# Optimization experiments

Measured on AMD Instinct MI355X. Metric: run time of the kernel, lower is better.

Reference implementation:

```python
import jax, jax.numpy as jnp
import numpy as np

N, NFEAT, NHID, NCLASS, NIDX = 200000, 512, 128, 70, 10000


def normalize_l2(X):
    # row L2-normalize; norm is detached in the original (stop_gradient),
    # inf scale (zero rows) mapped to 0
    rownorm = jax.lax.stop_gradient(jnp.linalg.norm(X, axis=1, keepdims=True))
    scale = jnp.where(rownorm > 0, 1.0 / rownorm, 0.0)
    return X * scale


def setup_inputs() -> dict:
    key = jax.random.key(0)
    ks = jax.random.split(key, 9)
    x = jax.random.normal(ks[0], (N, NFEAT), dtype=jnp.float32)
    simple_features = jax.random.normal(ks[1], (N, NFEAT), dtype=jnp.float32)
    idx = jax.random.randint(ks[2], (NIDX,), 0, N)
    s = 0.05
    W0 = jax.random.normal(ks[3], (NHID, NFEAT), dtype=jnp.float32) * s
    W1 = jax.random.normal(ks[4], (NHID, NFEAT), dtype=jnp.float32) * s
    G1 = jax.random.normal(ks[5], (NHID, NHID), dtype=jnp.float32) * s
    G2 = jax.random.normal(ks[6], (NHID, NHID), dtype=jnp.float32) * s
    GT = jax.random.normal(ks[7], (NHID, 2 * NHID), dtype=jnp.float32) * s
    Wc = jax.random.normal(ks[8], (NCLASS, NHID), dtype=jnp.float32) * s
    return {"x": x, "simple_features": simple_features, "idx": idx,
            "W0": W0, "W1": W1, "G1": G1, "G2": G2, "GT": GT, "Wc": Wc}


def reference(x, simple_features, idx, W0, W1, G1, G2, GT, Wc):
    x = normalize_l2(x)                      # [N, nfeat]
    sf = normalize_l2(simple_features)       # [N, nfeat]
    # dropout/dropout_adj are identity (p=0)
    layer_inner = jax.nn.relu(x @ W0.T)      # [N, nhid]
    lay_simple = jax.nn.relu(sf @ W1.T)      # [N, nhid]
    gate1 = layer_inner @ G1.T               # [N, nhid]
    gate2 = lay_simple @ G2.T                # [N, nhid]
    gate = jax.nn.sigmoid(jnp.concatenate([gate1, gate2], axis=1) @ GT.T)
    fix_inner = (1.0 - gate) * layer_inner + gate * lay_simple
    fix_inner = normalize_l2(fix_inner)
    logits = jax.nn.relu(fix_inner @ Wc.T)   # [N, nclass]
    return jax.nn.log_softmax(logits, axis=-1)[idx]
```

## Files before the change

### kernel.cpp

```cpp
#include <hip/hip_runtime.h>
#include <math.h>

#define NFEAT  512
#define NHID   128
#define NCLASS 70
#define NIDX   10000
#define NTILE  625
#define NT2    313
#define HELEMS (2u * NIDX * NHID)
#define GELEMS (2u * NIDX * NHID)
#define WIMG_ELEMS (2u * 128 * 512)
#define SMALL_ELEMS 74496u
#define WS_NEED ((size_t)(HELEMS + GELEMS + WIMG_ELEMS + SMALL_ELEMS) * 2)

typedef float  f32x4  __attribute__((ext_vector_type(4)));
typedef __bf16 bf16x8 __attribute__((ext_vector_type(8)));

static __device__ __forceinline__ unsigned short f2bf(float f) {
    unsigned u = __builtin_bit_cast(unsigned, f);
    u += 0x7fffu + ((u >> 16) & 1u);
    return (unsigned short)(u >> 16);
}
static __device__ __forceinline__ float bf2f(unsigned short h) {
    unsigned u = ((unsigned)h) << 16;
    return __builtin_bit_cast(float, u);
}
static __device__ __forceinline__ bf16x8 pack8(float4 a, float4 b) {
    bf16x8 r;
    r[0] = (__bf16)a.x; r[1] = (__bf16)a.y; r[2] = (__bf16)a.z; r[3] = (__bf16)a.w;
    r[4] = (__bf16)b.x; r[5] = (__bf16)b.y; r[6] = (__bf16)b.z; r[7] = (__bf16)b.w;
    return r;
}
static __device__ __forceinline__ bf16x8 pack8s(float4 a, float4 b, float s) {
    bf16x8 r;
    r[0] = (__bf16)(a.x * s); r[1] = (__bf16)(a.y * s); r[2] = (__bf16)(a.z * s); r[3] = (__bf16)(a.w * s);
    r[4] = (__bf16)(b.x * s); r[5] = (__bf16)(b.y * s); r[6] = (__bf16)(b.z * s); r[7] = (__bf16)(b.w * s);
    return r;
}
static __device__ __forceinline__ f32x4 MFMA(bf16x8 a, bf16x8 b, f32x4 c) {
    return __builtin_amdgcn_mfma_f32_16x16x32_bf16(a, b, c, 0, 0, 0);
}
static __device__ __forceinline__ bf16x8 ldsAx(const unsigned short* base, int row, int colb, int rstride) {
    return *(const bf16x8*)((const char*)base + row * rstride + (colb ^ ((row & 7) << 4)));
}
static __device__ __forceinline__ void ldsW1(unsigned short* base, int row, int col, unsigned short v) {
    *(unsigned short*)((char*)base + row * 256 + ((col * 2) ^ ((row & 7) << 4))) = v;
}
static __device__ __forceinline__ float ldsR1(const unsigned short* base, int row, int col) {
    return bf2f(*(const unsigned short*)((const char*)base + row * 256 + ((col * 2) ^ ((row & 7) << 4))));
}

__global__ void prep_weights(const float* __restrict__ W0, const float* __restrict__ W1,
                             const float* __restrict__ G1, const float* __restrict__ G2,
                             const float* __restrict__ GT, const float* __restrict__ Wc,
                             unsigned short* __restrict__ wsWimg,
                             unsigned short* __restrict__ wsSmall) {
    int i = blockIdx.x * 256 + threadIdx.x;
    if (i < 16384) {
        int t = i >> 13;
        int r = i & 8191;
        int n = r >> 6, k8 = r & 63;
        const float* src = (t ? W1 : W0) + (size_t)n * NFEAT + k8 * 8;
        float4 a = ((const float4*)src)[0], b = ((const float4*)src)[1];
        char* dst = (char*)wsWimg + t * 131072 + n * 1024 + ((k8 * 16) ^ ((n & 7) << 4));
        *(bf16x8*)dst = pack8(a, b);
    } else {
        int i4 = i - 16384;
        if (i4 >= 18624) return;
        const float* src; int base4, dstb;
        if      (i4 < 4096)  { src = G1; base4 = 0;     dstb = 0; }
        else if (i4 < 8192)  { src = G2; base4 = 4096;  dstb = 16384; }
        else if (i4 < 16384) { src = GT; base4 = 8192;  dstb = 32768; }
        else                 { src = Wc; base4 = 16384; dstb = 65536; }
        float4 v = ((const float4*)src)[i4 - base4];
        ushort4 o;
        o.x = f2bf(v.x); o.y = f2bf(v.y); o.z = f2bf(v.z); o.w = f2bf(v.w);
        *(ushort4*)(wsSmall + dstb + (size_t)(i4 - base4) * 4) = o;
    }
}

__global__ __launch_bounds__(512) void stageBC(
    const float* __restrict__ x, const float* __restrict__ sf,
    const int* __restrict__ idx,
    const unsigned short* __restrict__ wsWimg,
    const unsigned short* __restrict__ wsSmall,
    unsigned short* __restrict__ wsH,
    unsigned short* __restrict__ wsG)
{
    __shared__ __align__(16) unsigned short Wl[65536];
    __shared__ __align__(16) unsigned short Xl[8192];
    __shared__ __align__(16) unsigned short Hl[2048];
    __shared__ __align__(16) unsigned short Gl[2048];

    const int tid  = threadIdx.x;
    const int w    = tid >> 6;
    const int lane = tid & 63;
    const int ln   = lane & 15, lg = lane >> 4;
    const int bid  = blockIdx.x;
    const int t    = bid / 125, tb = bid % 125;
    const int tile0 = tb * 5;
    const float* XS = t ? sf : x;
    const f32x4 zero4 = {0.f, 0.f, 0.f, 0.f};

    float4 ga0, ga1, gb0, gb1;
    {
        int r0 = idx[tile0 * 16 + w];
        int r1 = idx[tile0 * 16 + w + 8];
        const float4* p0 = (const float4*)(XS + (size_t)r0 * NFEAT + lane * 8);
        const float4* p1 = (const float4*)(XS + (size_t)r1 * NFEAT + lane * 8);
        ga0 = p0[0]; ga1 = p0[1];
        gb0 = p1[0]; gb1 = p1[1];
    }
    bf16x8 cf[4];
    {
        const unsigned short* Gsm = wsSmall + t * 16384;
        #pragma unroll
        for (int kc = 0; kc < 4; ++kc)
            cf[kc] = *(const bf16x8*)(Gsm + (size_t)(w * 16 + ln) * NHID + kc * 32 + lg * 8);
    }
    {
        const uint4* src = (const uint4*)((const char*)wsWimg + (size_t)t * 131072);
        uint4* dst = (uint4*)Wl;
        #pragma unroll
        for (int i = 0; i < 16; ++i) dst[tid + i * 512] = src[tid + i * 512];
    }
    auto putX = [&](int m, float4 a, float4 b) {
        float ss = a.x*a.x + a.y*a.y + a.z*a.z + a.w*a.w
                 + b.x*b.x + b.y*b.y + b.z*b.z + b.w*b.w;
        #pragma unroll
        for (int d = 1; d < 64; d <<= 1) ss += __shfl_xor(ss, d);
        float scl = (ss > 0.f) ? (1.f / sqrtf(ss)) : 0.f;
        *(bf16x8*)((char*)Xl + m * 1024 + ((lane * 16) ^ ((m & 7) << 4))) = pack8s(a, b, scl);
    };
    putX(w,     ga0, ga1);
    putX(w + 8, gb0, gb1);
    __syncthreads();

    for (int it = 0; it < 5; ++it) {
        float4 na0, na1, nb0, nb1;
        if (it < 4) {
            int tile = tile0 + it + 1;
            int r0 = idx[tile * 16 + w];
            int r1 = idx[tile * 16 + w + 8];
            const float4* p0 = (const float4*)(XS + (size_t)r0 * NFEAT + lane * 8);
            const float4* p1 = (const float4*)(XS + (size_t)r1 * NFEAT + lane * 8);
            na0 = p0[0]; na1 = p0[1];
            nb0 = p1[0]; nb1 = p1[1];
        }
        f32x4 accE = zero4, accO = zero4;
        #pragma unroll
        for (int kc = 0; kc < 16; ++kc) {
            bf16x8 a = ldsAx(Xl, ln,          kc * 64 + lg * 16, 1024);
            bf16x8 b = ldsAx(Wl, w * 16 + ln, kc * 64 + lg * 16, 1024);
            if (kc & 1) accO = MFMA(a, b, accO); else accE = MFMA(a, b, accE);
        }
        f32x4 acc = accE + accO;
        #pragma unroll
        for (int rg = 0; rg < 4; ++rg)
            ldsW1(Hl, lg * 4 + rg, w * 16 + ln, f2bf(fmaxf(acc[rg], 0.f)));
        __syncthreads();

        f32x4 aC = zero4;
        #pragma unroll
        for (int kc = 0; kc < 4; ++kc) {
            bf16x8 a = ldsAx(Hl, ln, kc * 64 + lg * 16, 256);
            aC = MFMA(a, cf[kc], aC);
        }
        if (tid < 256) {
            int tile = tile0 + it;
            ((uint4*)(wsH + ((size_t)t * NIDX + (size_t)tile * 16) * NHID))[tid]
                = ((const uint4*)Hl)[tid];
        }
        if (it < 4) {
            putX(w,     na0, na1);
            putX(w + 8, nb0, nb1);
        }
        #pragma unroll
        for (int rg = 0; rg < 4; ++rg)
            ldsW1(Gl, lg * 4 + rg, w * 16 + ln, f2bf(aC[rg]));
        __syncthreads();

        if (tid < 256) {
            int tile = tile0 + it;
            ((uint4*)(wsG + ((size_t)t * NIDX + (size_t)tile * 16) * NHID))[tid]
                = ((const uint4*)Gl)[tid];
        }
    }
}

__global__ __launch_bounds__(512) void tailDE2(
    const unsigned short* __restrict__ wsSmall,
    const unsigned short* __restrict__ wsH,
    const unsigned short* __restrict__ wsG,
    float* __restrict__ out)
{
    __shared__ __align__(16) unsigned short Hbuf[2][2][16][NHID];
    __shared__ __align__(16) unsigned short G12s[2][2][16][NHID];
    __shared__ __align__(16) unsigned short FIXs[2][16][NHID];
    __shared__ float scl2[2][16];

    const unsigned short* GTp = wsSmall + 32768;
    const unsigned short* Wcp = wsSmall + 65536;

    const int tid  = threadIdx.x;
    const int bid  = blockIdx.x;
    const int w    = tid >> 6;
    const int lane = tid & 63;
    const int ln   = lane & 15, lg = lane >> 4;
    const f32x4 zero4 = {0.f, 0.f, 0.f, 0.f};
    const int tile0 = bid * 2;
    const int tiles[2] = { tile0, (tile0 + 1 < NTILE) ? tile0 + 1 : NTILE - 1 };

    #pragma unroll
    for (int i = 0; i < 2; ++i) {
        int q = tid + i * 512;
        int seg = q >> 8, r = q & 255;
        int ti = seg >> 1, tt = seg & 1;
        size_t off = ((size_t)tt * NIDX + (size_t)tiles[ti] * 16) * NHID;
        ((uint4*)&Hbuf[0][0][0][0])[q] = ((const uint4*)(wsH + off))[r];
        ((uint4*)&G12s[0][0][0][0])[q] = ((const uint4*)(wsG + off))[r];
    }
    const int nD = w * 16 + ln;
    bf16x8 gt[8];
    #pragma unroll
    for (int kc = 0; kc < 8; ++kc)
        gt[kc] = *(const bf16x8*)(GTp + (size_t)nD * (2 * NHID) + kc * 32 + lg * 8);
    const int ccE = w * 16 + ln;
    const int ccl = (ccE < NCLASS) ? ccE : 0;
    bf16x8 wcf[4];
    #pragma unroll
    for (int kc = 0; kc < 4; ++kc)
        wcf[kc] = *(const bf16x8*)(Wcp + (size_t)ccl * NHID + kc * 32 + lg * 8);
    __syncthreads();

    #pragma unroll
    for (int ti = 0; ti < 2; ++ti) {
        f32x4 aE = zero4, aO = zero4;
        #pragma unroll
        for (int kc = 0; kc < 8; ++kc) {
            const unsigned short* As = &G12s[ti][kc >> 2][0][0];
            bf16x8 a = ldsAx(As, ln, (kc & 3) * 64 + lg * 16, 256);
            if (kc & 1) aO = MFMA(a, gt[kc], aO); else aE = MFMA(a, gt[kc], aE);
        }
        f32x4 accD = aE + aO;
        #pragma unroll
        for (int rg = 0; rg < 4; ++rg) {
            int m = lg * 4 + rg;
            float g  = 1.f / (1.f + __expf(-accD[rg]));
            float h0 = ldsR1(&Hbuf[ti][0][0][0], m, nD);
            float h1 = ldsR1(&Hbuf[ti][1][0][0], m, nD);
            ldsW1(&FIXs[ti][0][0], m, nD, f2bf((1.f - g) * h0 + g * h1));
        }
    }
    __syncthreads();

    {
        int rr = tid >> 4, sl = tid & 15;
        int ti = rr >> 4, r = rr & 15;
        bf16x8 v = ldsAx(&FIXs[ti][0][0], r, sl * 16, 256);
        float ss = 0.f;
        #pragma unroll
        for (int j = 0; j < 8; ++j) { float f = (float)v[j]; ss += f * f; }
        ss += __shfl_xor(ss, 1); ss += __shfl_xor(ss, 2);
        ss += __shfl_xor(ss, 4); ss += __shfl_xor(ss, 8);
        if (sl == 0) scl2[ti][r] = (ss > 0.f) ? (1.f / sqrtf(ss)) : 0.f;
    }
    __syncthreads();

    if (w < 5) {
        const bool live = (ccE < NCLASS);
        bf16x8 bfz;
        #pragma unroll
        for (int j = 0; j < 8; ++j) bfz[j] = (__bf16)0.f;
        #pragma unroll
        for (int ti = 0; ti < 2; ++ti) {
            f32x4 accE = zero4;
            #pragma unroll
            for (int kc = 0; kc < 4; ++kc) {
                bf16x8 a = ldsAx(&FIXs[ti][0][0], ln, kc * 64 + lg * 16, 256);
                accE = MFMA(a, live ? wcf[kc] : bfz, accE);
            }
            if (live) {
                float* LO = (float*)((char*)&G12s[0][0][0][0] + ti * 8192);
                #pragma unroll
                for (int rg = 0; rg < 4; ++rg) {
                    int m = lg * 4 + rg;
                    LO[m * 80 + ccE] = fmaxf(accE[rg] * scl2[ti][m], 0.f);
                }
            }
        }
    }
    __syncthreads();

    {
        int rr = tid >> 4, l16 = tid & 15;
        int ti = rr >> 4, r = rr & 15;
        const float* LO = (const float*)((const char*)&G12s[0][0][0][0] + ti * 8192) + r * 80;
        float v[5];
        #pragma unroll
        for (int j = 0; j < 5; ++j) {
            int c = l16 + j * 16;
            v[j] = (c < NCLASS) ? LO[c] : -1e30f;
        }
        float mx = v[0];
        #pragma unroll
        for (int j = 1; j < 5; ++j) mx = fmaxf(mx, v[j]);
        mx = fmaxf(mx, __shfl_xor(mx, 1)); mx = fmaxf(mx, __shfl_xor(mx, 2));
        mx = fmaxf(mx, __shfl_xor(mx, 4)); mx = fmaxf(mx, __shfl_xor(mx, 8));
        float se = 0.f;
        #pragma unroll
        for (int j = 0; j < 5; ++j) {
            int c = l16 + j * 16;
            if (c < NCLASS) se += __expf(v[j] - mx);
        }
        se += __shfl_xor(se, 1); se += __shfl_xor(se, 2);
        se += __shfl_xor(se, 4); se += __shfl_xor(se, 8);
        float lz = mx + __logf(se);
        int tile = tile0 + ti;
        if (tile < NTILE) {
            size_t orow = (size_t)tile * 16 + r;
            #pragma unroll
            for (int j = 0; j < 5; ++j) {
                int c = l16 + j * 16;
                if (c < NCLASS) out[orow * NCLASS + c] = v[j] - lz;
            }
        }
    }
}

static __device__ __forceinline__ bf16x8 bfragF(const float* p, size_t off) {
    const float4* q = (const float4*)(p + off);
    return pack8(q[0], q[1]);
}
__global__ __launch_bounds__(512) void hyper_fb(
    const float* __restrict__ x, const float* __restrict__ sf,
    const int* __restrict__ idx,
    const float* __restrict__ W0, const float* __restrict__ W1,
    const float* __restrict__ G1, const float* __restrict__ G2,
    const float* __restrict__ GT, const float* __restrict__ Wc,
    float* __restrict__ out)
{
    __shared__ __align__(16) unsigned short Xbuf[2][16][NFEAT];
    __shared__ __align__(16) unsigned short Hbuf[2][16][NHID];
    __shared__ float scl2[16];
    unsigned short* G12 = &Xbuf[0][0][0];
    unsigned short* FIX = &Xbuf[0][0][0] + 4096;
    float*          LOG = (float*)(&Xbuf[0][0][0] + 6144);

    const int tid = threadIdx.x, bid = blockIdx.x;
    const int w = tid >> 6, lane = tid & 63;
    const int ln = lane & 15, lg = lane >> 4;
    const int tB = w >> 2, nq = w & 3;
    const f32x4 zero4 = {0.f, 0.f, 0.f, 0.f};

    {
        char* xb = (char*)&Xbuf[0][0][0];
        #pragma unroll
        for (int j = 0; j < 4; ++j) {
            int p = w * 4 + j, t = p >> 4, m = p & 15;
            int ri = idx[bid * 16 + m];
            const float4* q = (const float4*)((t ? sf : x) + (size_t)ri * NFEAT + lane * 8);
            float4 a = q[0], b = q[1];
            float ss = a.x*a.x + a.y*a.y + a.z*a.z + a.w*a.w
                     + b.x*b.x + b.y*b.y + b.z*b.z + b.w*b.w;
            #pragma unroll
            for (int d = 1; d < 64; d <<= 1) ss += __shfl_xor(ss, d);
            float scl = (ss > 0.f) ? (1.f / sqrtf(ss)) : 0.f;
            int soff = t * 16384 + m * 1024 + ((lane * 16) ^ ((m & 7) << 4));
            *(bf16x8*)(xb + soff) = pack8s(a, b, scl);
        }
    }
    __syncthreads();
    {
        const float* Wp = tB ? W1 : W0;
        f32x4 acc0 = zero4, acc1 = zero4;
        const unsigned short* Xb = (const unsigned short*)((const char*)&Xbuf[0][0][0] + tB * 16384);
        #pragma unroll
        for (int kc = 0; kc < 16; ++kc) {
            bf16x8 a = ldsAx(Xb, ln, kc * 64 + lg * 16, 1024);
            acc0 = MFMA(a, bfragF(Wp, (size_t)(nq * 32 + ln) * NFEAT + kc * 32 + lg * 8), acc0);
            acc1 = MFMA(a, bfragF(Wp, (size_t)(nq * 32 + 16 + ln) * NFEAT + kc * 32 + lg * 8), acc1);
        }
        unsigned short* Hb = &Hbuf[tB][0][0];
        #pragma unroll
        for (int rg = 0; rg < 4; ++rg) {
            int m = lg * 4 + rg;
            ldsW1(Hb, m, nq * 32 + ln,      f2bf(fmaxf(acc0[rg], 0.f)));
            ldsW1(Hb, m, nq * 32 + 16 + ln, f2bf(fmaxf(acc1[rg], 0.f)));
        }
    }
    __syncthreads();
    {
        const float* Gp = tB ? G2 : G1;
        const unsigned short* Hs = &Hbuf[tB][0][0];
        f32x4 accC[2] = {zero4, zero4};
        #pragma unroll
        for (int kc = 0; kc < 4; ++kc) {
            bf16x8 a = ldsAx(Hs, ln, kc * 64 + lg * 16, 256);
            accC[0] = MFMA(a, bfragF(Gp, (size_t)(nq * 32 + ln) * NHID + kc * 32 + lg * 8), accC[0]);
            accC[1] = MFMA(a, bfragF(Gp, (size_t)(nq * 32 + 16 + ln) * NHID + kc * 32 + lg * 8), accC[1]);
        }
        unsigned short* Gd = G12 + tB * 2048;
        #pragma unroll
        for (int nt = 0; nt < 2; ++nt)
            #pragma unroll
            for (int rg = 0; rg < 4; ++rg) {
                int m = lg * 4 + rg;
                ldsW1(Gd, m, nq * 32 + nt * 16 + ln, f2bf(accC[nt][rg]));
            }
    }
    __syncthreads();
    {
        f32x4 accD = zero4;
        const int n = w * 16 + ln;
        #pragma unroll
        for (int kc = 0; kc < 8; ++kc) {
            const unsigned short* As = G12 + (kc >> 2) * 2048;
            bf16x8 a = ldsAx(As, ln, (kc & 3) * 64 + lg * 16, 256);
            accD = MFMA(a, bfragF(GT, (size_t)n * (2 * NHID) + kc * 32 + lg * 8), accD);
        }
        #pragma unroll
        for (int rg = 0; rg < 4; ++rg) {
            int m = lg * 4 + rg;
            float g  = 1.f / (1.f + __expf(-accD[rg]));
            float h0 = ldsR1(&Hbuf[0][0][0], m, n);
            float h1 = ldsR1(&Hbuf[1][0][0], m, n);
            ldsW1(FIX, m, n, f2bf((1.f - g) * h0 + g * h1));
        }
    }
    __syncthreads();
    if (tid < 256) {
        int r = tid >> 4, sl = tid & 15;
        bf16x8 v = ldsAx(FIX, r, sl * 16, 256);
        float ss = 0.f;
        #pragma unroll
        for (int j = 0; j < 8; ++j) { float f = (float)v[j]; ss += f * f; }
        ss += __shfl_xor(ss, 1); ss += __shfl_xor(ss, 2);
        ss += __shfl_xor(ss, 4); ss += __shfl_xor(ss, 8);
        if (sl == 0) scl2[r] = (ss > 0.f) ? (1.f / sqrtf(ss)) : 0.f;
    }
    __syncthreads();
    if (w < 5) {
        const int cc = w * 16 + ln;
        bf16x8 bfz;
        #pragma unroll
        for (int j = 0; j < 8; ++j) bfz[j] = (__bf16)0.f;
        f32x4 accE = zero4;
        #pragma unroll
        for (int kc = 0; kc < 4; ++kc) {
            bf16x8 a = ldsAx(FIX, ln, kc * 64 + lg * 16, 256);
            bf16x8 b = (cc < NCLASS) ? bfragF(Wc, (size_t)cc * NHID + kc * 32 + lg * 8) : bfz;
            accE = MFMA(a, b, accE);
        }
        #pragma unroll
        for (int rg = 0; rg < 4; ++rg) {
            int m = lg * 4 + rg;
            float v = fmaxf(accE[rg] * scl2[m], 0.f);
            LOG[m * 80 + cc] = (cc < NCLASS) ? v : -1e30f;
        }
    }
    __syncthreads();
    {
        const int r = tid >> 5, l32 = tid & 31;
        float v0 = LOG[r * 80 + l32];
        float v1 = LOG[r * 80 + 32 + l32];
        float v2 = (l32 < 16) ? LOG[r * 80 + 64 + l32] : -1e30f;
        float mx = fmaxf(fmaxf(v0, v1), v2);
        #pragma unroll
        for (int d = 1; d < 32; d <<= 1) mx = fmaxf(mx, __shfl_xor(mx, d, 32));
        float se = __expf(v0 - mx) + __expf(v1 - mx) + ((l32 < 16) ? __expf(v2 - mx) : 0.f);
        #pragma unroll
        for (int d = 1; d < 32; d <<= 1) se += __shfl_xor(se, d, 32);
        float lz = mx + __logf(se);
        size_t orow = (size_t)bid * 16 + r;
        out[orow * NCLASS + l32] = v0 - lz;
        if (l32 + 32 < NCLASS) out[orow * NCLASS + 32 + l32] = v1 - lz;
        if (l32 + 64 < NCLASS) out[orow * NCLASS + 64 + l32] = v2 - lz;
    }
}

extern "C" void kernel_launch(void* const* d_in, const int* in_sizes, int n_in,
                              void* d_out, int out_size, void* d_ws, size_t ws_size,
                              hipStream_t stream)
{
    const float* x   = (const float*)d_in[0];
    const float* sf  = (const float*)d_in[1];
    const int*   idx = (const int*)d_in[2];
    const float* W0  = (const float*)d_in[3];
    const float* W1  = (const float*)d_in[4];
    const float* G1  = (const float*)d_in[5];
    const float* G2  = (const float*)d_in[6];
    const float* GT  = (const float*)d_in[7];
    const float* Wc  = (const float*)d_in[8];
    float* out = (float*)d_out;

    if (ws_size >= WS_NEED) {
        unsigned short* wsH     = (unsigned short*)d_ws;
        unsigned short* wsG     = wsH + HELEMS;
        unsigned short* wsWimg  = wsG + GELEMS;
        unsigned short* wsSmall = wsWimg + WIMG_ELEMS;
        prep_weights<<<dim3(137), dim3(256), 0, stream>>>(W0, W1, G1, G2, GT, Wc, wsWimg, wsSmall);
        stageBC<<<dim3(250), dim3(512), 0, stream>>>(x, sf, idx, wsWimg, wsSmall, wsH, wsG);
        tailDE2<<<dim3(NT2), dim3(512), 0, stream>>>(wsSmall, wsH, wsG, out);
    } else {
        hyper_fb<<<dim3(NTILE), dim3(512), 0, stream>>>(
            x, sf, idx, W0, W1, G1, G2, GT, Wc, out);
    }
}
```

Before: 36.95 us.

## Fuse tail stage into stageBC via last-arriver atomic counter per tile group

```diff
diff --git a/kernel.cpp b/kernel.cpp
--- a/kernel.cpp
+++ b/kernel.cpp
@@ -6,12 +6,12 @@
 #define NCLASS 70
 #define NIDX   10000
 #define NTILE  625
-#define NT2    313
 #define HELEMS (2u * NIDX * NHID)
 #define GELEMS (2u * NIDX * NHID)
 #define WIMG_ELEMS (2u * 128 * 512)
 #define SMALL_ELEMS 74496u
-#define WS_NEED ((size_t)(HELEMS + GELEMS + WIMG_ELEMS + SMALL_ELEMS) * 2)
+#define CNT_OFF ((size_t)(HELEMS + GELEMS + WIMG_ELEMS + SMALL_ELEMS) * 2)
+#define WS_NEED (CNT_OFF + 512)
 
 typedef float  f32x4  __attribute__((ext_vector_type(4)));
 typedef __bf16 bf16x8 __attribute__((ext_vector_type(8)));
@@ -79,18 +79,24 @@
     }
 }
 
-__global__ __launch_bounds__(512) void stageBC(
+__global__ __launch_bounds__(512) void hyperFused(
     const float* __restrict__ x, const float* __restrict__ sf,
     const int* __restrict__ idx,
     const unsigned short* __restrict__ wsWimg,
     const unsigned short* __restrict__ wsSmall,
     unsigned short* __restrict__ wsH,
-    unsigned short* __restrict__ wsG)
+    unsigned short* __restrict__ wsG,
+    int* __restrict__ cnt,
+    float* __restrict__ out)
 {
-    __shared__ __align__(16) unsigned short Wl[65536];
-    __shared__ __align__(16) unsigned short Xl[8192];
-    __shared__ __align__(16) unsigned short Hl[2048];
-    __shared__ __align__(16) unsigned short Gl[2048];
+    __shared__ __align__(16) char SM[155648];
+    __shared__ float scl2s[5][16];
+    __shared__ int wflag;
+
+    unsigned short* Wl = (unsigned short*)SM;
+    unsigned short* Xl = (unsigned short*)(SM + 131072);
+    unsigned short* Hl = (unsigned short*)(SM + 147456);
+    unsigned short* Gl = (unsigned short*)(SM + 151552);
 
     const int tid  = threadIdx.x;
     const int w    = tid >> 6;
@@ -186,59 +192,50 @@
                 = ((const uint4*)Gl)[tid];
         }
     }
-}
-
-__global__ __launch_bounds__(512) void tailDE2(
-    const unsigned short* __restrict__ wsSmall,
-    const unsigned short* __restrict__ wsH,
-    const unsigned short* __restrict__ wsG,
-    float* __restrict__ out)
-{
-    __shared__ __align__(16) unsigned short Hbuf[2][2][16][NHID];
-    __shared__ __align__(16) unsigned short G12s[2][2][16][NHID];
-    __shared__ __align__(16) unsigned short FIXs[2][16][NHID];
-    __shared__ float scl2[2][16];
-
+
+    const int nD = w * 16 + ln;
     const unsigned short* GTp = wsSmall + 32768;
     const unsigned short* Wcp = wsSmall + 65536;
-
-    const int tid  = threadIdx.x;
-    const int bid  = blockIdx.x;
-    const int w    = tid >> 6;
-    const int lane = tid & 63;
-    const int ln   = lane & 15, lg = lane >> 4;
-    const f32x4 zero4 = {0.f, 0.f, 0.f, 0.f};
-    const int tile0 = bid * 2;
-    const int tiles[2] = { tile0, (tile0 + 1 < NTILE) ? tile0 + 1 : NTILE - 1 };
-
-    #pragma unroll
-    for (int i = 0; i < 2; ++i) {
-        int q = tid + i * 512;
-        int seg = q >> 8, r = q & 255;
-        int ti = seg >> 1, tt = seg & 1;
-        size_t off = ((size_t)tt * NIDX + (size_t)tiles[ti] * 16) * NHID;
-        ((uint4*)&Hbuf[0][0][0][0])[q] = ((const uint4*)(wsH + off))[r];
-        ((uint4*)&G12s[0][0][0][0])[q] = ((const uint4*)(wsG + off))[r];
-    }
-    const int nD = w * 16 + ln;
     bf16x8 gt[8];
     #pragma unroll
     for (int kc = 0; kc < 8; ++kc)
         gt[kc] = *(const bf16x8*)(GTp + (size_t)nD * (2 * NHID) + kc * 32 + lg * 8);
-    const int ccE = w * 16 + ln;
+    const int ccE = nD;
     const int ccl = (ccE < NCLASS) ? ccE : 0;
     bf16x8 wcf[4];
     #pragma unroll
     for (int kc = 0; kc < 4; ++kc)
         wcf[kc] = *(const bf16x8*)(Wcp + (size_t)ccl * NHID + kc * 32 + lg * 8);
-    __syncthreads();
+
+    __threadfence();
+    __syncthreads();
+    if (tid == 0) wflag = atomicAdd(&cnt[tb], 1);
+    __syncthreads();
+    if (wflag != 1) return;
+    __threadfence();
+
+    unsigned short* Hb = (unsigned short*)SM;
+    unsigned short* Gb = (unsigned short*)(SM + 40960);
+    unsigned short* FX = (unsigned short*)(SM + 81920);
+    float* LOGb = (float*)SM;
 
     #pragma unroll
-    for (int ti = 0; ti < 2; ++ti) {
+    for (int i = 0; i < 5; ++i) {
+        int q = tid + i * 512;
+        int seg = q >> 8, r = q & 255;
+        int ti = seg >> 1, tt = seg & 1;
+        size_t off = ((size_t)tt * NIDX + (size_t)(tile0 + ti) * 16) * NHID;
+        ((uint4*)Hb)[q] = ((const uint4*)(wsH + off))[r];
+        ((uint4*)Gb)[q] = ((const uint4*)(wsG + off))[r];
+    }
+    __syncthreads();
+
+    #pragma unroll
+    for (int ti = 0; ti < 5; ++ti) {
         f32x4 aE = zero4, aO = zero4;
         #pragma unroll
         for (int kc = 0; kc < 8; ++kc) {
-            const unsigned short* As = &G12s[ti][kc >> 2][0][0];
+            const unsigned short* As = Gb + ti * 4096 + (kc >> 2) * 2048;
             bf16x8 a = ldsAx(As, ln, (kc & 3) * 64 + lg * 16, 256);
             if (kc & 1) aO = MFMA(a, gt[kc], aO); else aE = MFMA(a, gt[kc], aE);
         }
@@ -247,23 +244,29 @@
         for (int rg = 0; rg < 4; ++rg) {
             int m = lg * 4 + rg;
             float g  = 1.f / (1.f + __expf(-accD[rg]));
-            float h0 = ldsR1(&Hbuf[ti][0][0][0], m, nD);
-            float h1 = ldsR1(&Hbuf[ti][1][0][0], m, nD);
-            ldsW1(&FIXs[ti][0][0], m, nD, f2bf((1.f - g) * h0 + g * h1));
+            float h0 = ldsR1(Hb + ti * 4096,        m, nD);
+            float h1 = ldsR1(Hb + ti * 4096 + 2048, m, nD);
+            ldsW1(FX + ti * 2048, m, nD, f2bf((1.f - g) * h0 + g * h1));
         }
     }
     __syncthreads();
 
     {
         int rr = tid >> 4, sl = tid & 15;
-        int ti = rr >> 4, r = rr & 15;
-        bf16x8 v = ldsAx(&FIXs[ti][0][0], r, sl * 16, 256);
-        float ss = 0.f;
-        #pragma unroll
-        for (int j = 0; j < 8; ++j) { float f = (float)v[j]; ss += f * f; }
-        ss += __shfl_xor(ss, 1); ss += __shfl_xor(ss, 2);
-        ss += __shfl_xor(ss, 4); ss += __shfl_xor(ss, 8);
-        if (sl == 0) scl2[ti][r] = (ss > 0.f) ? (1.f / sqrtf(ss)) : 0.f;
+        #pragma unroll
+        for (int j = 0; j < 3; ++j) {
+            int rs = j * 32 + rr;
+            if (rs < 80) {
+                int ti = rs >> 4, r = rs & 15;
+                bf16x8 v = ldsAx(FX + ti * 2048, r, sl * 16, 256);
+                float ss = 0.f;
+                #pragma unroll
+                for (int jj = 0; jj < 8; ++jj) { float f = (float)v[jj]; ss += f * f; }
+                ss += __shfl_xor(ss, 1); ss += __shfl_xor(ss, 2);
+                ss += __shfl_xor(ss, 4); ss += __shfl_xor(ss, 8);
+                if (sl == 0) scl2s[ti][r] = (ss > 0.f) ? (1.f / sqrtf(ss)) : 0.f;
+            }
+        }
     }
     __syncthreads();
 
@@ -273,19 +276,19 @@
         #pragma unroll
         for (int j = 0; j < 8; ++j) bfz[j] = (__bf16)0.f;
         #pragma unroll
-        for (int ti = 0; ti < 2; ++ti) {
+        for (int ti = 0; ti < 5; ++ti) {
             f32x4 accE = zero4;
             #pragma unroll
             for (int kc = 0; kc < 4; ++kc) {
-                bf16x8 a = ldsAx(&FIXs[ti][0][0], ln, kc * 64 + lg * 16, 256);
+                bf16x8 a = ldsAx(FX + ti * 2048, ln, kc * 64 + lg * 16, 256);
                 accE = MFMA(a, live ? wcf[kc] : bfz, accE);
             }
             if (live) {
-                float* LO = (float*)((char*)&G12s[0][0][0][0] + ti * 8192);
+                float* LO = LOGb + ti * 1280;
                 #pragma unroll
                 for (int rg = 0; rg < 4; ++rg) {
                     int m = lg * 4 + rg;
-                    LO[m * 80 + ccE] = fmaxf(accE[rg] * scl2[ti][m], 0.f);
+                    LO[m * 80 + ccE] = fmaxf(accE[rg] * scl2s[ti][m], 0.f);
                 }
             }
         }
@@ -294,35 +297,38 @@
 
     {
         int rr = tid >> 4, l16 = tid & 15;
-        int ti = rr >> 4, r = rr & 15;
-        const float* LO = (const float*)((const char*)&G12s[0][0][0][0] + ti * 8192) + r * 80;
-        float v[5];
-        #pragma unroll
-        for (int j = 0; j < 5; ++j) {
-            int c = l16 + j * 16;
-            v[j] = (c < NCLASS) ? LO[c] : -1e30f;
-        }
-        float mx = v[0];
-        #pragma unroll
-        for (int j = 1; j < 5; ++j) mx = fmaxf(mx, v[j]);
-        mx = fmaxf(mx, __shfl_xor(mx, 1)); mx = fmaxf(mx, __shfl_xor(mx, 2));
-        mx = fmaxf(mx, __shfl_xor(mx, 4)); mx = fmaxf(mx, __shfl_xor(mx, 8));
-        float se = 0.f;
-        #pragma unroll
-        for (int j = 0; j < 5; ++j) {
-            int c = l16 + j * 16;
-            if (c < NCLASS) se += __expf(v[j] - mx);
-        }
-        se += __shfl_xor(se, 1); se += __shfl_xor(se, 2);
-        se += __shfl_xor(se, 4); se += __shfl_xor(se, 8);
-        float lz = mx + __logf(se);
-        int tile = tile0 + ti;
-        if (tile < NTILE) {
-            size_t orow = (size_t)tile * 16 + r;
-            #pragma unroll
-            for (int j = 0; j < 5; ++j) {
-                int c = l16 + j * 16;
-                if (c < NCLASS) out[orow * NCLASS + c] = v[j] - lz;
+        #pragma unroll
+        for (int j = 0; j < 3; ++j) {
+            int rs = j * 32 + rr;
+            if (rs < 80) {
+                int ti = rs >> 4, r = rs & 15;
+                const float* LO = LOGb + ti * 1280 + r * 80;
+                float v[5];
+                #pragma unroll
+                for (int jj = 0; jj < 5; ++jj) {
+                    int c = l16 + jj * 16;
+                    v[jj] = (c < NCLASS) ? LO[c] : -1e30f;
+                }
+                float mx = v[0];
+                #pragma unroll
+                for (int jj = 1; jj < 5; ++jj) mx = fmaxf(mx, v[jj]);
+                mx = fmaxf(mx, __shfl_xor(mx, 1)); mx = fmaxf(mx, __shfl_xor(mx, 2));
+                mx = fmaxf(mx, __shfl_xor(mx, 4)); mx = fmaxf(mx, __shfl_xor(mx, 8));
+                float se = 0.f;
+                #pragma unroll
+                for (int jj = 0; jj < 5; ++jj) {
+                    int c = l16 + jj * 16;
+                    if (c < NCLASS) se += __expf(v[jj] - mx);
+                }
+                se += __shfl_xor(se, 1); se += __shfl_xor(se, 2);
+                se += __shfl_xor(se, 4); se += __shfl_xor(se, 8);
+                float lz = mx + __logf(se);
+                size_t orow = (size_t)(tile0 + ti) * 16 + r;
+                #pragma unroll
+                for (int jj = 0; jj < 5; ++jj) {
+                    int c = l16 + jj * 16;
+                    if (c < NCLASS) out[orow * NCLASS + c] = v[jj] - lz;
+                }
             }
         }
     }
@@ -499,9 +505,11 @@
         unsigned short* wsG     = wsH + HELEMS;
         unsigned short* wsWimg  = wsG + GELEMS;
         unsigned short* wsSmall = wsWimg + WIMG_ELEMS;
+        int* cnt = (int*)((char*)d_ws + CNT_OFF);
+        hipMemsetAsync(cnt, 0, 128 * sizeof(int), stream);
         prep_weights<<<dim3(137), dim3(256), 0, stream>>>(W0, W1, G1, G2, GT, Wc, wsWimg, wsSmall);
-        stageBC<<<dim3(250), dim3(512), 0, stream>>>(x, sf, idx, wsWimg, wsSmall, wsH, wsG);
-        tailDE2<<<dim3(NT2), dim3(512), 0, stream>>>(wsSmall, wsH, wsG, out);
+        hyperFused<<<dim3(250), dim3(512), 0, stream>>>(
+            x, sf, idx, wsWimg, wsSmall, wsH, wsG, cnt, out);
     } else {
         hyper_fb<<<dim3(NTILE), dim3(512), 0, stream>>>(
             x, sf, idx, W0, W1, G1, G2, GT, Wc, out);
```

Result: slower. 98.24 us (+165.9%).
